# Optimization experiments

Measured on AMD Instinct MI355X. Metric: run time of the kernel, lower is better.

Reference implementation:

```python
import jax, jax.numpy as jnp
import numpy as np

B, K, L = 8, 288, 16384   # K = C*kh*kw = 32*3*3
O = 64                    # output channels


def setup_inputs() -> dict:
    key = jax.random.key(0)
    k1, k2, k3 = jax.random.split(key, 3)
    x_unf = jax.random.normal(k1, (B, K, L), dtype=jnp.float32)
    w = jax.random.normal(k2, (O, 32, 3, 3), dtype=jnp.float32)
    b = jax.random.normal(k3, (O,), dtype=jnp.float32)
    gamma = jnp.float32(0.005)
    return {"x_unf": x_unf, "w": w, "b": b, "gamma": gamma}


def reference(x_unf, w, b, gamma):
    # torch: l = x_unf.transpose(1,2)[:,:,:,None] - w.view(1,1,-1,w.size(0))
    #        l = sum(l**2, dim=2); t = exp(-gamma*l) + b
    o = w.shape[0]
    wv = jnp.reshape(w, (-1,))            # row-major flatten, same as torch .view
    wv = jnp.reshape(wv, (-1, o))         # [K, O] (memory reinterpretation, NOT transpose)
    xt = jnp.transpose(x_unf, (0, 2, 1))  # [B, L, K]
    x2 = jnp.sum(xt * xt, axis=-1, keepdims=True)       # [B, L, 1]
    w2 = jnp.sum(wv * wv, axis=0)[None, None, :]        # [1, 1, O]
    xw = jnp.einsum('blk,ko->blo', xt, wv)              # [B, L, O]
    d2 = x2 + w2 - 2.0 * xw                             # [B, L, O]
    t = jnp.exp(-gamma * d2)
    return t + b
```

## Files before the change

kernel.cpp:

```cpp
#include <hip/hip_runtime.h>

#define LDIM 16384
#define KDIM 288
#define ODIM 64
#define BDIM 8

typedef float f32x4 __attribute__((ext_vector_type(4)));
typedef short bf16x8 __attribute__((ext_vector_type(8)));

__device__ __forceinline__ short f2bf(float f) {
  unsigned u = __builtin_bit_cast(unsigned, f);
  unsigned r = u + 0x7FFFu + ((u >> 16) & 1u);
  return (short)(r >> 16);
}

__global__ __launch_bounds__(256) void gauss_pre(const float* __restrict__ w,
                                                 const float* __restrict__ gammap,
                                                 short* __restrict__ wfrag,
                                                 float* __restrict__ cw) {
  int tid = threadIdx.x;
  int blk = blockIdx.x;

  if (blk < 9) {
    int kc = blk;
    int ln = tid & 63;
    int nt = tid >> 6;
    int k0 = kc * 32 + (ln >> 4) * 8;
    int n = nt * 16 + (ln & 15);
    bf16x8 v;
#pragma unroll
    for (int j = 0; j < 8; ++j) v[j] = f2bf(w[(k0 + j) * 64 + n]);
    *(bf16x8*)(wfrag + ((kc * 4 + nt) * 64 + ln) * 8) = v;
  } else {
    __shared__ float red[256];
    int o = tid & 63;
    int seg = tid >> 6;
    float s = 0.f;
#pragma unroll 8
    for (int k = seg * 72; k < seg * 72 + 72; ++k) {
      float v = w[k * 64 + o];
      s = fmaf(v, v, s);
    }
    red[tid] = s;
    __syncthreads();
    if (tid < 64) {
      float t = red[tid] + red[tid + 64] + red[tid + 128] + red[tid + 192];
      cw[tid] = -gammap[0] * t;
    }
  }
}

__global__ __launch_bounds__(256, 4) void gauss_main(
    const float* __restrict__ x, const short* __restrict__ wfrag,
    const float* __restrict__ cw, const float* __restrict__ bias,
    const float* __restrict__ gammap, float* __restrict__ out) {
  const int t = threadIdx.x;
  const int lane = t & 63;
  const int wvid = t >> 6;
  const int m = lane & 15;
  const int g = lane >> 4;

  const long g0 = (long)blockIdx.x * 128;
  const int bidx = (int)(g0 >> 14);
  const int l0 = (int)(g0 & (LDIM - 1));

  const float* xc = x + (long)bidx * ((long)KDIM * LDIM) +
                    (long)(g * 8) * LDIM + (l0 + wvid * 32 + m);

  float xv0[8], xv1[8], nx0[8], nx1[8];
#pragma unroll
  for (int j = 0; j < 8; ++j) {
    xv0[j] = xc[(long)j * LDIM];
    xv1[j] = xc[(long)j * LDIM + 16];
  }

  const f32x4 zero = {0.f, 0.f, 0.f, 0.f};
  f32x4 acc[2][4];
#pragma unroll
  for (int tt = 0; tt < 2; ++tt)
#pragma unroll
    for (int nt = 0; nt < 4; ++nt) acc[tt][nt] = zero;
  float x2a[2] = {0.f, 0.f};

#pragma unroll 1
  for (int kc = 0; kc < 9; ++kc) {
    if (kc < 8) {
      const float* nxp = xc + (long)((kc + 1) * 32) * LDIM;
#pragma unroll
      for (int j = 0; j < 8; ++j) {
        nx0[j] = nxp[(long)j * LDIM];
        nx1[j] = nxp[(long)j * LDIM + 16];
      }
    }

    const short* wp = wfrag + ((kc * 4) * 64 + lane) * 8;
    bf16x8 bfr[4];
#pragma unroll
    for (int nt = 0; nt < 4; ++nt) bfr[nt] = *(const bf16x8*)(wp + nt * 512);

    bf16x8 a0, a1;
#pragma unroll
    for (int j = 0; j < 8; ++j) {
      x2a[0] = fmaf(xv0[j], xv0[j], x2a[0]);
      a0[j] = f2bf(xv0[j]);
    }
#pragma unroll
    for (int j = 0; j < 8; ++j) {
      x2a[1] = fmaf(xv1[j], xv1[j], x2a[1]);
      a1[j] = f2bf(xv1[j]);
    }

#pragma unroll
    for (int nt = 0; nt < 4; ++nt) {
      acc[0][nt] = __builtin_amdgcn_mfma_f32_16x16x32_bf16(a0, bfr[nt], acc[0][nt], 0, 0, 0);
      acc[1][nt] = __builtin_amdgcn_mfma_f32_16x16x32_bf16(a1, bfr[nt], acc[1][nt], 0, 0, 0);
    }

    if (kc < 8) {
#pragma unroll
      for (int j = 0; j < 8; ++j) {
        xv0[j] = nx0[j];
        xv1[j] = nx1[j];
      }
    }
  }

#pragma unroll
  for (int tt = 0; tt < 2; ++tt) {
    x2a[tt] += __shfl_xor(x2a[tt], 16, 64);
    x2a[tt] += __shfl_xor(x2a[tt], 32, 64);
  }

  const float gamma = gammap[0];
  const float coef = 2.f * gamma;
  float cwv[4], bv[4];
#pragma unroll
  for (int nt = 0; nt < 4; ++nt) {
    cwv[nt] = cw[nt * 16 + m];
    bv[nt] = bias[nt * 16 + m];
  }

  float* ob = out + (g0 + wvid * 32) * 64;
#pragma unroll
  for (int tt = 0; tt < 2; ++tt) {
#pragma unroll
    for (int r = 0; r < 4; ++r) {
      int row = g * 4 + r;
      float x2v = __shfl(x2a[tt], (lane & 48) | row, 64);
      float cx = -gamma * x2v;
      int lrow = tt * 16 + row;
#pragma unroll
      for (int nt = 0; nt < 4; ++nt) {
        float e = fmaf(coef, acc[tt][nt][r], cx + cwv[nt]);
        ob[lrow * 64 + nt * 16 + m] = __expf(e) + bv[nt];
      }
    }
  }
}

extern "C" void kernel_launch(void* const* d_in, const int* in_sizes, int n_in,
                              void* d_out, int out_size, void* d_ws, size_t ws_size,
                              hipStream_t stream) {
  const float* x = (const float*)d_in[0];
  const float* w = (const float*)d_in[1];
  const float* b = (const float*)d_in[2];
  const float* gamma = (const float*)d_in[3];
  float* out = (float*)d_out;

  short* wfrag = (short*)d_ws;
  float* cw = (float*)((char*)d_ws + 36864);

  gauss_pre<<<10, 256, 0, stream>>>(w, gamma, wfrag, cw);
  gauss_main<<<1024, 256, 0, stream>>>(x, wfrag, cw, b, gamma, out);
}
```

Measured before the change: 232.6 us.

## Fuse weight prep into main kernel and stage x via async global-to-LDS loads

Merges the weight-fragment and |w|^2 precompute kernel into the main kernel, so each block converts weights to bf16 into LDS itself and the separate launch goes away. x tiles are now double-buffered in LDS through global_load_lds DMA with a swizzled layout, and explicit vmcnt waits plus barriers replace the per-thread register prefetch. Every one of the 1024 blocks now redoes the weight conversion and reduction from global memory, and the occupancy hint drops from 4 to 2 blocks per CU because of the larger LDS footprint.

```diff
diff --git a/kernel.cpp b/kernel.cpp
--- a/kernel.cpp
+++ b/kernel.cpp
@@ -14,46 +14,14 @@
   return (short)(r >> 16);
 }
 
-__global__ __launch_bounds__(256) void gauss_pre(const float* __restrict__ w,
-                                                 const float* __restrict__ gammap,
-                                                 short* __restrict__ wfrag,
-                                                 float* __restrict__ cw) {
-  int tid = threadIdx.x;
-  int blk = blockIdx.x;
+__global__ __launch_bounds__(256, 2) void gauss_all(
+    const float* __restrict__ x, const float* __restrict__ w,
+    const float* __restrict__ bias, const float* __restrict__ gammap,
+    float* __restrict__ out) {
+  __shared__ float xs[2][4096];
+  __shared__ short wlds[36 * 512];
+  __shared__ float red[256];
 
-  if (blk < 9) {
-    int kc = blk;
-    int ln = tid & 63;
-    int nt = tid >> 6;
-    int k0 = kc * 32 + (ln >> 4) * 8;
-    int n = nt * 16 + (ln & 15);
-    bf16x8 v;
-#pragma unroll
-    for (int j = 0; j < 8; ++j) v[j] = f2bf(w[(k0 + j) * 64 + n]);
-    *(bf16x8*)(wfrag + ((kc * 4 + nt) * 64 + ln) * 8) = v;
-  } else {
-    __shared__ float red[256];
-    int o = tid & 63;
-    int seg = tid >> 6;
-    float s = 0.f;
-#pragma unroll 8
-    for (int k = seg * 72; k < seg * 72 + 72; ++k) {
-      float v = w[k * 64 + o];
-      s = fmaf(v, v, s);
-    }
-    red[tid] = s;
-    __syncthreads();
-    if (tid < 64) {
-      float t = red[tid] + red[tid + 64] + red[tid + 128] + red[tid + 192];
-      cw[tid] = -gammap[0] * t;
-    }
-  }
-}
-
-__global__ __launch_bounds__(256, 4) void gauss_main(
-    const float* __restrict__ x, const short* __restrict__ wfrag,
-    const float* __restrict__ cw, const float* __restrict__ bias,
-    const float* __restrict__ gammap, float* __restrict__ out) {
   const int t = threadIdx.x;
   const int lane = t & 63;
   const int wvid = t >> 6;
@@ -63,15 +31,70 @@
   const long g0 = (long)blockIdx.x * 128;
   const int bidx = (int)(g0 >> 14);
   const int l0 = (int)(g0 & (LDIM - 1));
+  const float* xb = x + (long)bidx * ((long)KDIM * LDIM) + l0;
 
-  const float* xc = x + (long)bidx * ((long)KDIM * LDIM) +
-                    (long)(g * 8) * LDIM + (l0 + wvid * 32 + m);
+  const float* sp[4];
+#pragma unroll
+  for (int i = 0; i < 4; ++i) {
+    int s = wvid * 4 + i;
+    int k = s * 2 + (lane >> 5);
+    int l4s = ((lane & 31) - 2 * (k >> 3)) & 31;
+    sp[i] = xb + (long)k * LDIM + l4s * 4;
+  }
 
-  float xv0[8], xv1[8], nx0[8], nx1[8];
+#define STAGE(KC, BUF)                                                        \
+  {                                                                           \
+    _Pragma("unroll") for (int i = 0; i < 4; ++i) {                           \
+      __builtin_amdgcn_global_load_lds(                                       \
+          (const __attribute__((address_space(1))) unsigned int*)(void*)      \
+              (sp[i] + (long)(KC) * 32 * LDIM),                               \
+          (__attribute__((address_space(3))) unsigned int*)(void*)            \
+              (&xs[BUF][(wvid * 4 + i) * 256]),                               \
+          16, 0, 0);                                                          \
+    }                                                                         \
+  }
+
+  STAGE(0, 0)
+  STAGE(1, 1)
+
 #pragma unroll
-  for (int j = 0; j < 8; ++j) {
-    xv0[j] = xc[(long)j * LDIM];
-    xv1[j] = xc[(long)j * LDIM + 16];
+  for (int q = 0; q < 9; ++q) {
+    int rr = wvid + q * 4;
+    int kcw = rr >> 2, nt = rr & 3;
+    int k0 = kcw * 32 + g * 8;
+    int n = nt * 16 + m;
+    bf16x8 v;
+#pragma unroll
+    for (int j = 0; j < 8; ++j) v[j] = f2bf(w[(k0 + j) * 64 + n]);
+    *(bf16x8*)(wlds + rr * 512 + lane * 8) = v;
+  }
+
+  const float gamma = gammap[0];
+  {
+    const int seg = t >> 6, o = t & 63;
+    float s = 0.f;
+#pragma unroll 8
+    for (int k = seg * 72; k < seg * 72 + 72; ++k) {
+      float v = w[k * 64 + o];
+      s = fmaf(v, v, s);
+    }
+    red[t] = s;
+  }
+  __syncthreads();
+
+  float cwv[4], bv[4];
+#pragma unroll
+  for (int nt = 0; nt < 4; ++nt) {
+    int col = nt * 16 + m;
+    cwv[nt] = -gamma * (red[col] + red[col + 64] + red[col + 128] + red[col + 192]);
+    bv[nt] = bias[col];
+  }
+
+  int ab[2];
+#pragma unroll
+  for (int tt = 0; tt < 2; ++tt) {
+    int l = wvid * 32 + tt * 16 + m;
+    ab[tt] = g * 4096 + ((((l >> 2) + 2 * g) & 31) * 16) + (l & 3) * 4;
   }
 
   const f32x4 zero = {0.f, 0.f, 0.f, 0.f};
@@ -82,48 +105,36 @@
     for (int nt = 0; nt < 4; ++nt) acc[tt][nt] = zero;
   float x2a[2] = {0.f, 0.f};
 
+#define COMPUTE(KC)                                                           \
+  {                                                                           \
+    const char* xbase = (const char*)&xs[(KC) & 1][0];                        \
+    bf16x8 bfr[4];                                                            \
+    _Pragma("unroll") for (int nt = 0; nt < 4; ++nt)                          \
+        bfr[nt] = *(const bf16x8*)(wlds + ((KC) * 4 + nt) * 512 + lane * 8);  \
+    _Pragma("unroll") for (int tt = 0; tt < 2; ++tt) {                        \
+      const float* ap = (const float*)(xbase + ab[tt]);                       \
+      float a[8];                                                             \
+      bf16x8 afr;                                                             \
+      _Pragma("unroll") for (int j = 0; j < 8; ++j) a[j] = ap[j * 128];       \
+      _Pragma("unroll") for (int j = 0; j < 8; ++j) {                         \
+        x2a[tt] = fmaf(a[j], a[j], x2a[tt]);                                  \
+        afr[j] = f2bf(a[j]);                                                  \
+      }                                                                       \
+      _Pragma("unroll") for (int nt = 0; nt < 4; ++nt)                        \
+          acc[tt][nt] = __builtin_amdgcn_mfma_f32_16x16x32_bf16(              \
+              afr, bfr[nt], acc[tt][nt], 0, 0, 0);                            \
+    }                                                                         \
+  }
+
 #pragma unroll 1
-  for (int kc = 0; kc < 9; ++kc) {
-    if (kc < 8) {
-      const float* nxp = xc + (long)((kc + 1) * 32) * LDIM;
-#pragma unroll
-      for (int j = 0; j < 8; ++j) {
-        nx0[j] = nxp[(long)j * LDIM];
-        nx1[j] = nxp[(long)j * LDIM + 16];
-      }
-    }
-
-    const short* wp = wfrag + ((kc * 4) * 64 + lane) * 8;
-    bf16x8 bfr[4];
-#pragma unroll
-    for (int nt = 0; nt < 4; ++nt) bfr[nt] = *(const bf16x8*)(wp + nt * 512);
-
-    bf16x8 a0, a1;
-#pragma unroll
-    for (int j = 0; j < 8; ++j) {
-      x2a[0] = fmaf(xv0[j], xv0[j], x2a[0]);
-      a0[j] = f2bf(xv0[j]);
-    }
-#pragma unroll
-    for (int j = 0; j < 8; ++j) {
-      x2a[1] = fmaf(xv1[j], xv1[j], x2a[1]);
-      a1[j] = f2bf(xv1[j]);
-    }
-
-#pragma unroll
-    for (int nt = 0; nt < 4; ++nt) {
-      acc[0][nt] = __builtin_amdgcn_mfma_f32_16x16x32_bf16(a0, bfr[nt], acc[0][nt], 0, 0, 0);
-      acc[1][nt] = __builtin_amdgcn_mfma_f32_16x16x32_bf16(a1, bfr[nt], acc[1][nt], 0, 0, 0);
-    }
-
-    if (kc < 8) {
-#pragma unroll
-      for (int j = 0; j < 8; ++j) {
-        xv0[j] = nx0[j];
-        xv1[j] = nx1[j];
-      }
-    }
+  for (int kc = 0; kc < 8; ++kc) {
+    asm volatile("s_waitcnt vmcnt(4)" ::: "memory");
+    COMPUTE(kc)
+    __builtin_amdgcn_s_barrier();
+    if (kc < 7) STAGE(kc + 2, kc & 1)
   }
+  asm volatile("s_waitcnt vmcnt(0)" ::: "memory");
+  COMPUTE(8)
 
 #pragma unroll
   for (int tt = 0; tt < 2; ++tt) {
@@ -131,15 +142,7 @@
     x2a[tt] += __shfl_xor(x2a[tt], 32, 64);
   }
 
-  const float gamma = gammap[0];
   const float coef = 2.f * gamma;
-  float cwv[4], bv[4];
-#pragma unroll
-  for (int nt = 0; nt < 4; ++nt) {
-    cwv[nt] = cw[nt * 16 + m];
-    bv[nt] = bias[nt * 16 + m];
-  }
-
   float* ob = out + (g0 + wvid * 32) * 64;
 #pragma unroll
   for (int tt = 0; tt < 2; ++tt) {
@@ -156,6 +159,8 @@
       }
     }
   }
+#undef STAGE
+#undef COMPUTE
 }
 
 extern "C" void kernel_launch(void* const* d_in, const int* in_sizes, int n_in,
@@ -167,9 +172,6 @@
   const float* gamma = (const float*)d_in[3];
   float* out = (float*)d_out;
 
-  short* wfrag = (short*)d_ws;
-  float* cw = (float*)((char*)d_ws + 36864);
-
-  gauss_pre<<<10, 256, 0, stream>>>(w, gamma, wfrag, cw);
-  gauss_main<<<1024, 256, 0, stream>>>(x, wfrag, cw, b, gamma, out);
+  (void)d_ws; (void)ws_size;
+  gauss_all<<<1024, 256, 0, stream>>>(x, w, b, gamma, out);
 }
```

New measurement: 228.5 us. No clear change (-1.8%).
